# Performance work log

Measured on AMD Instinct MI355X. Metric: run time of the kernel, lower is better.

Reference implementation:

```python
import jax, jax.numpy as jnp
import numpy as np

K, D, N = 32, 128, 65536
EPS = 1e-6


def setup_inputs() -> dict:
    key = jax.random.key(0)
    k1, k2, k3 = jax.random.split(key, 3)
    x = jax.random.normal(k1, (N, D), dtype=jnp.float32)
    means = jax.random.normal(k2, (K, D), dtype=jnp.float32)
    # SPD covariances (original init is identity; use SPD perturbation so Cholesky is valid)
    B = jax.random.normal(k3, (K, D, D), dtype=jnp.float32) * 0.1
    covariances = jnp.einsum('kij,klj->kil', B, B) / D + jnp.eye(D, dtype=jnp.float32)
    weights = jnp.ones((K,), dtype=jnp.float32) / K
    return {"x": x, "means": means, "covariances": covariances, "weights": weights}


def reference(x, means, covariances, weights):
    d = x.shape[-1]
    cov = covariances + EPS * jnp.eye(d, dtype=x.dtype)          # [K,D,D]
    L = jnp.linalg.cholesky(cov)                                 # [K,D,D]
    diff = x[None, :, :] - means[:, None, :]                     # [K,N,D]
    # Mahalanobis via triangular solve: m = ||L^{-1}(x-mu)||^2
    sol = jax.scipy.linalg.solve_triangular(
        L, jnp.swapaxes(diff, 1, 2), lower=True)                 # [K,D,N]
    maha = jnp.sum(sol * sol, axis=1)                            # [K,N]
    half_logdet = jnp.sum(jnp.log(jnp.diagonal(L, axis1=1, axis2=2)), axis=1)  # [K]
    log_prob = (-0.5 * (d * jnp.log(2.0 * jnp.pi) + maha)
                - half_logdet[:, None])                          # [K,N]
    weighted = log_prob.T + jnp.log(weights)                     # [N,K]
    return jax.nn.logsumexp(weighted, axis=1)                    # [N]
```

## Files before the change

### kernel.cpp

```cpp
#include <hip/hip_runtime.h>
#include <hip/hip_bf16.h>
#include <math.h>

#define KCOMP 32
#define DDIM  128
#define NPTS  65536
#define GMM_EPS 1e-6f
#define SA 129
#define UFT 1280

typedef __attribute__((ext_vector_type(8)))  __bf16 bf16x8;
typedef __attribute__((ext_vector_type(16))) float  f32x16;

__device__ __forceinline__ unsigned short f2bf(float f){
  unsigned u = __builtin_bit_cast(unsigned, f);
  u = (u + 0x7FFFu + ((u >> 16) & 1u)) >> 16;
  return (unsigned short)u;
}
__device__ __forceinline__ float rlane(float v, int lsrc){
  return __builtin_bit_cast(float, __builtin_amdgcn_readlane(__builtin_bit_cast(int, v), lsrc));
}

__device__ __noinline__ float chol_inv32(float* __restrict__ Ab,
                                         float* __restrict__ Wb,
                                         const int c){
  float ar[32], lr[32], rd[32], s[32];
  #pragma unroll
  for(int i=0;i<32;i++) ar[i] = Ab[i*SA + c];
  float mydiag = 1.f;
  #pragma unroll
  for(int j=0;j<32;j++){
    float d   = rlane(ar[j], j);
    float rsd = rsqrtf(d);
    rd[j] = rsd;
    float Lcj  = ar[j]*rsd;
    lr[j] = (c>=j) ? Lcj : 0.f;
    if(c==j) mydiag = Lcj;
    float coef = Lcj*rsd;
    #pragma unroll
    for(int i=j+1;i<32;i++){
      float bij = rlane(ar[i], j);
      ar[i] = fmaf(-bij, coef, ar[i]);
    }
  }
  #pragma unroll
  for(int j=0;j<32;j++) Ab[c*SA + j] = lr[j];
  #pragma unroll
  for(int i=0;i<32;i++) s[i] = (i==c) ? 1.f : 0.f;
  #pragma unroll
  for(int j=0;j<32;j++){
    float vj = s[j]*rd[j];
    s[j] = vj;
    #pragma unroll
    for(int i=j+1;i<32;i++)
      s[i] = fmaf(-rlane(lr[j], i), vj, s[i]);
  }
  #pragma unroll
  for(int i=0;i<32;i++) Wb[i*SA + c] = s[i];
  return logf(mydiag);
}

__device__ __noinline__ void panel_unit(float* __restrict__ A, const float* __restrict__ W,
                                        int r0, int c0, int b, int ibl){
  const int b32=b*32;
  float acc[4][4]={};
  for(int kc=0;kc<32;kc+=4){
    float a_[4][4], b_[4][4];
    #pragma unroll
    for(int e=0;e<4;e++)
      #pragma unroll
      for(int g=0;g<4;g++){
        a_[e][g]=A[(32*ibl+r0+e)*SA + b32+kc+g];
        b_[e][g]=W[(b32+c0+e)*SA   + b32+kc+g];
      }
    #pragma unroll
    for(int e=0;e<4;e++)
      #pragma unroll
      for(int f=0;f<4;f++)
        acc[e][f]+=a_[e][0]*b_[f][0]+a_[e][1]*b_[f][1]
                  +a_[e][2]*b_[f][2]+a_[e][3]*b_[f][3];
  }
  #pragma unroll
  for(int e=0;e<4;e++)
    #pragma unroll
    for(int f=0;f<4;f++)
      A[(32*ibl+r0+e)*SA + b32+c0+f] = acc[e][f];
}

__device__ __noinline__ void syrk_unit(float* __restrict__ A,
                                       int r0, int c0, int b, int ui, int uj){
  const int b32=b*32;
  float acc[4][4]={};
  for(int kc=0;kc<32;kc+=4){
    float a_[4][4], b_[4][4];
    #pragma unroll
    for(int e=0;e<4;e++)
      #pragma unroll
      for(int g=0;g<4;g++){
        a_[e][g]=A[(32*ui+r0+e)*SA + b32+kc+g];
        b_[e][g]=A[(32*uj+c0+e)*SA + b32+kc+g];
      }
    #pragma unroll
    for(int e=0;e<4;e++)
      #pragma unroll
      for(int f=0;f<4;f++)
        acc[e][f]+=a_[e][0]*b_[f][0]+a_[e][1]*b_[f][1]
                  +a_[e][2]*b_[f][2]+a_[e][3]*b_[f][3];
  }
  #pragma unroll
  for(int e=0;e<4;e++)
    #pragma unroll
    for(int f=0;f<4;f++)
      A[(32*ui+r0+e)*SA+32*uj+c0+f] -= acc[e][f];
}

__device__ __noinline__ void tg_unit(const float* __restrict__ A, const float* __restrict__ W,
                                     float* __restrict__ T, int r0, int c0, int i, int j){
  float acc[4][4]={};
  #pragma unroll 1
  for(int p=j;p<i;p++){
    for(int kc=0;kc<32;kc+=4){
      float a_[4][4], b_[4][4];
      #pragma unroll
      for(int e=0;e<4;e++)
        #pragma unroll
        for(int g=0;g<4;g++){
          a_[e][g]=A[(32*i+r0+e)*SA + 32*p+kc+g];
          b_[e][g]=W[(32*p+kc+e)*SA + 32*j+c0+g];
        }
      #pragma unroll
      for(int e=0;e<4;e++)
        #pragma unroll
        for(int f=0;f<4;f++)
          acc[e][f]+=a_[e][0]*b_[0][f]+a_[e][1]*b_[1][f]
                    +a_[e][2]*b_[2][f]+a_[e][3]*b_[3][f];
    }
  }
  #pragma unroll
  for(int e=0;e<4;e++)
    #pragma unroll
    for(int f=0;f<4;f++)
      T[(r0+e)*33+c0+f]=acc[e][f];
}

__device__ __noinline__ void a2_unit(float* __restrict__ W, const float* __restrict__ T,
                                     int r0, int c0, int i, int j){
  float ac2[4][4]={};
  for(int kc=0;kc<32;kc+=4){
    float a_[4][4], b_[4][4];
    #pragma unroll
    for(int e=0;e<4;e++)
      #pragma unroll
      for(int g=0;g<4;g++){
        a_[e][g]=W[(32*i+r0+e)*SA + 32*i+kc+g];
        b_[e][g]=T[(kc+e)*33 + c0+g];
      }
    #pragma unroll
    for(int e=0;e<4;e++)
      #pragma unroll
      for(int f=0;f<4;f++)
        ac2[e][f]+=a_[e][0]*b_[0][f]+a_[e][1]*b_[1][f]
                  +a_[e][2]*b_[2][f]+a_[e][3]*b_[3][f];
  }
  #pragma unroll
  for(int e=0;e<4;e++)
    #pragma unroll
    for(int f=0;f<4;f++)
      W[(32*i+r0+e)*SA+32*j+c0+f] = -ac2[e][f];
}

__device__ __forceinline__ void pack_tile(const float* __restrict__ W,
                                          uint4* __restrict__ uf4, int tile, int l){
  int db = (tile<2)?0:((tile<6)?1:((tile<12)?2:3));
  int kc = tile - ((db==0)?0:((db==1)?2:((db==2)?6:12)));
  int row=db*32+(l&31), colb=kc*16+((l>>5)<<3);
  unsigned uu[4];
  #pragma unroll
  for(int h2=0;h2<4;h2++){
    unsigned lo=f2bf(W[row*SA+colb+2*h2]);
    unsigned hi=f2bf(W[row*SA+colb+2*h2+1]);
    uu[h2]=lo|(hi<<16);
  }
  uint4 wv; wv.x=uu[0]; wv.y=uu[1]; wv.z=uu[2]; wv.w=uu[3];
  uf4[tile*64 + l] = wv;
}

__global__ __launch_bounds__(256) void k_prep(const float* __restrict__ cov,
                                              const float* __restrict__ wts,
                                              const float* __restrict__ means,
                                              float* __restrict__ ws_c3,
                                              unsigned short* __restrict__ qfrag,
                                              unsigned short* __restrict__ ufrag){
  __shared__ float A[DDIM*SA];
  __shared__ float W[DDIM*SA];
  __shared__ float Tb[3*1056];
  __shared__ float muS[DDIM];
  __shared__ float mq[256];
  const int t=threadIdx.x, w=t>>6, l=t&63, k=blockIdx.x;
  const int r0=(l>>3)*4, c0=(l&7)*4;
  uint4* ufK = (uint4*)ufrag + (size_t)k*UFT;

  const float4* cv4 = (const float4*)(cov + (size_t)k*DDIM*DDIM);
  #pragma unroll
  for(int v=0; v<16; v++){
    int idx4 = t + 256*v; float4 f = cv4[idx4];
    int e = idx4*4; int i = e>>7; int j = e&127;
    float* d = &A[i*SA+j]; d[0]=f.x; d[1]=f.y; d[2]=f.z; d[3]=f.w;
  }
  for(int z=t; z<DDIM*SA; z+=256) W[z] = 0.f;
  if(t<DDIM) muS[t] = means[k*DDIM+t];
  __syncthreads();
  if(t<DDIM) A[t*SA+t] += GMM_EPS;
  __syncthreads();

  float hl = 0.f;
  if(w==0) hl += chol_inv32(&A[0], &W[0], l&31);
  __syncthreads();
  if(w==1)      panel_unit(A,W,r0,c0,0,1);
  else if(w==2) panel_unit(A,W,r0,c0,0,2);
  else if(w==3) panel_unit(A,W,r0,c0,0,3);
  __syncthreads();
  if(w==0)      syrk_unit(A,r0,c0,0,1,1);
  else if(w==1) syrk_unit(A,r0,c0,0,2,1);
  else if(w==2) syrk_unit(A,r0,c0,0,3,1);
  else          syrk_unit(A,r0,c0,0,2,2);
  __syncthreads();
  if(w==0)      hl += chol_inv32(&A[32*SA+32], &W[32*SA+32], l&31);
  else if(w==1) syrk_unit(A,r0,c0,0,3,2);
  else if(w==2) syrk_unit(A,r0,c0,0,3,3);
  __syncthreads();
  if(w==1)      panel_unit(A,W,r0,c0,1,2);
  else if(w==2) panel_unit(A,W,r0,c0,1,3);
  else if(w==3) tg_unit(A,W,&Tb[0],r0,c0,1,0);
  __syncthreads();
  if(w==0)      syrk_unit(A,r0,c0,1,2,2);
  else if(w==1) a2_unit(W,&Tb[0],r0,c0,1,0);
  else if(w==2) tg_unit(A,W,&Tb[1056],r0,c0,2,1);
  else          syrk_unit(A,r0,c0,1,3,2);
  __syncthreads();
  if(w==0)      hl += chol_inv32(&A[64*SA+64], &W[64*SA+64], l&31);
  else if(w==1) syrk_unit(A,r0,c0,1,3,3);
  else if(w==2) tg_unit(A,W,&Tb[0],r0,c0,2,0);
  __syncthreads();
  if(w==1)      panel_unit(A,W,r0,c0,2,3);
  else if(w==2) a2_unit(W,&Tb[0],r0,c0,2,0);
  else if(w==3) a2_unit(W,&Tb[1056],r0,c0,2,1);
  __syncthreads();
  if(w==0)      syrk_unit(A,r0,c0,2,3,3);
  else if(w==1) tg_unit(A,W,&Tb[0],r0,c0,3,0);
  else if(w==2) tg_unit(A,W,&Tb[1056],r0,c0,3,1);
  else          tg_unit(A,W,&Tb[2112],r0,c0,3,2);
  __syncthreads();
  if(w==0)      hl += chol_inv32(&A[96*SA+96], &W[96*SA+96], l&31);
  else if(w==1 || (w==2 && l<32)){
    int r = (w==1)? l : 64+l;
    float s=0.f;
    #pragma unroll 8
    for(int c=0;c<DDIM;c++) s += W[r*SA+c]*muS[c];
    mq[r]=s;
  }
  __syncthreads();
  if(w==1)      a2_unit(W,&Tb[0],r0,c0,3,0);
  else if(w==2) a2_unit(W,&Tb[1056],r0,c0,3,1);
  else if(w==3) a2_unit(W,&Tb[2112],r0,c0,3,2);
  __syncthreads();
  if(w==0){
    if(l<32){
      int r = 96+l;
      float s=0.f;
      #pragma unroll 8
      for(int c=0;c<DDIM;c++) s += W[r*SA+c]*muS[c];
      mq[r]=s;
    }
  } else {
    #pragma unroll
    for(int j=0;j<4;j++) pack_tile(W, ufK, (w-1)*4+j, l);
  }
  __syncthreads();
  if(t<128){
    float s=0.f;
    #pragma unroll 8
    for(int r=0;r<DDIM;r++) s += W[r*SA+t]*mq[r];
    mq[128+t]=s;
  } else if(w==2){
    #pragma unroll
    for(int j=0;j<4;j++) pack_tile(W, ufK, 12+j, l);
  } else {
    #pragma unroll
    for(int j=0;j<4;j++) pack_tile(W, ufK, 16+j, l);
  }
  __syncthreads();
  if(w==0){
    float hv = (l<32)? hl : 0.f;
    float p  = mq[l]*mq[l] + mq[l+64]*mq[l+64];
    #pragma unroll
    for(int off=32; off; off>>=1){ hv += __shfl_xor(hv,off); p += __shfl_xor(p,off); }
    if(l==0) ws_c3[k] = logf(wts[k]) - hv - 117.6241322f - 0.5f*p;
  } else if(w==1 && l<16){
    int tile=l>>1, half=l&1;
    const float* qq=&mq[128 + tile*16 + half*8];
    unsigned uu[4];
    #pragma unroll
    for(int h2=0;h2<4;h2++){
      unsigned lo=f2bf(qq[2*h2]), hi=f2bf(qq[2*h2+1]);
      uu[h2]=lo|(hi<<16);
    }
    uint4 wv; wv.x=uu[0]; wv.y=uu[1]; wv.z=uu[2]; wv.w=uu[3];
    ((uint4*)qfrag)[tile*64 + half*32 + k] = wv;
  }
}

#define MFMA_B(acc,u,xv) acc=__builtin_amdgcn_mfma_f32_32x32x16_bf16(__builtin_bit_cast(bf16x8,u),xv,acc,0,0,0)

__global__ __launch_bounds__(512,2) void k_main(const float* __restrict__ x,
                                                const uint4* __restrict__ uf,
                                                const uint4* __restrict__ qf,
                                                const float* __restrict__ ws_c3,
                                                float* __restrict__ out){
  __shared__ uint4 xs[4*8*64];
  __shared__ float lin[KCOMP*128];
  __shared__ float mahaS[4*8*128];
  __shared__ float c3s[KCOMP];
  const int t=threadIdx.x, lane=t&63, w=t>>6;
  const int qh=lane>>5, ln=lane&31;
  const size_t n0=(size_t)blockIdx.x*128;

  if(t<KCOMP) c3s[t]=ws_c3[t];

  {
    const float* xb = x + n0*DDIM;
    #pragma unroll
    for(int j=0;j<8;j++){
      int idx = j*512 + t;
      int n = idx & 127, d0 = (idx>>7)*4;
      float4 f = *(const float4*)(xb + (size_t)n*DDIM + d0);
      unsigned lo = f2bf(f.x) | (((unsigned)f2bf(f.y))<<16);
      unsigned hi = f2bf(f.z) | (((unsigned)f2bf(f.w))<<16);
      int tile=n>>5, lnn=n&31, c=d0>>4, qq=(d0>>3)&1, e4=d0&7;
      *(uint2*)((char*)xs + tile*8192 + c*1024 + qq*512 + lnn*16 + e4*2)
          = make_uint2(lo,hi);
    }
  }
  __syncthreads();

  if(w<4){
    f32x16 aq={};
    #pragma unroll
    for(int c=0;c<8;c++){
      uint4 qr = qf[c*64+lane];
      bf16x8 xq = __builtin_bit_cast(bf16x8, xs[w*512 + c*64 + lane]);
      MFMA_B(aq, qr, xq);
    }
    #pragma unroll
    for(int r=0;r<16;r++){
      int row=(r&3)+8*(r>>2)+4*qh;
      lin[row*128 + w*32 + ln] = -2.f*aq[r];
    }
  }

  #pragma unroll 1
  for(int iter=0;iter<4;iter++){
    const int k = iter*8 + w;
    uint4 ur[20];
    #pragma unroll
    for(int j=0;j<20;j++) ur[j]=uf[(size_t)k*UFT + j*64 + lane];

    #pragma unroll 1
    for(int tile=0;tile<4;tile++){
      bf16x8 xf[8];
      #pragma unroll
      for(int c=0;c<8;c++) xf[c]=__builtin_bit_cast(bf16x8, xs[tile*512 + c*64 + lane]);
      f32x16 a0={},a1={},a2={},a3={};
      #pragma unroll
      for(int c=0;c<2;c++) MFMA_B(a0, ur[c],    xf[c]);
      #pragma unroll
      for(int c=0;c<4;c++) MFMA_B(a1, ur[2+c],  xf[c]);
      #pragma unroll
      for(int c=0;c<6;c++) MFMA_B(a2, ur[6+c],  xf[c]);
      #pragma unroll
      for(int c=0;c<8;c++) MFMA_B(a3, ur[12+c], xf[c]);
      float p0=0.f,p1=0.f,p2=0.f,p3=0.f;
      #pragma unroll
      for(int r=0;r<16;r+=2){
        p0=fmaf(a0[r],a0[r],p0); p1=fmaf(a0[r+1],a0[r+1],p1);
        p2=fmaf(a1[r],a1[r],p2); p3=fmaf(a1[r+1],a1[r+1],p3);
        p0=fmaf(a2[r],a2[r],p0); p1=fmaf(a2[r+1],a2[r+1],p1);
        p2=fmaf(a3[r],a3[r],p2); p3=fmaf(a3[r+1],a3[r+1],p3);
      }
      float p=(p0+p1)+(p2+p3);
      p += __shfl_xor(p,32);
      if(qh==0) mahaS[iter*1024 + w*128 + tile*32 + ln] = p;
    }
  }
  __syncthreads();

  if(t<128){
    float m_run=-INFINITY, s_run=0.f;
    #pragma unroll 1
    for(int k3=0;k3<KCOMP;k3++){
      float a  = c3s[k3] - 0.5f*(mahaS[(k3>>3)*1024 + (k3&7)*128 + t] + lin[k3*128 + t]);
      float nm = fmaxf(m_run,a);
      s_run = s_run*__expf(m_run-nm)+__expf(a-nm);
      m_run = nm;
    }
    out[n0+t] = m_run + logf(s_run);
  }
}

extern "C" void kernel_launch(void* const* d_in, const int* in_sizes, int n_in,
                              void* d_out, int out_size, void* d_ws, size_t ws_size,
                              hipStream_t stream){
  const float* x   = (const float*)d_in[0];
  const float* mu  = (const float*)d_in[1];
  const float* cov = (const float*)d_in[2];
  const float* wts = (const float*)d_in[3];
  float* out = (float*)d_out;
  char*  ws  = (char*)d_ws;

  float*          wsC3 = (float*)ws;
  unsigned short* wsQF = (unsigned short*)(ws + 512);
  unsigned short* wsUF = (unsigned short*)(ws + 16384);

  k_prep<<<KCOMP, 256, 0, stream>>>(cov, wts, mu, wsC3, wsQF, wsUF);
  k_main<<<NPTS/128, 512, 0, stream>>>(x, (const uint4*)wsUF, (const uint4*)wsQF, wsC3, out);
}
```

Measured before the change: 174.4 us.

## Split per-component MFMA chains across wave pairs to halve register use

Each component's four triangular accumulator chains are now split between two waves: one wave handles the 2- and 8-chunk chains, the other the 4- and 6-chunk chains. This balances MFMA work and halves the preloaded U fragments per wave (10 instead of 20). Partial Mahalanobis sums are combined with shared-memory atomic adds into a zero-initialised buffer. Launch bounds are raised to 4 blocks per CU to increase occupancy. The trade-off is that U fragments are reloaded per component, shared atomics are added, and register pressure under the new bound may force spills.

```diff
diff --git a/kernel.cpp b/kernel.cpp
--- a/kernel.cpp
+++ b/kernel.cpp
@@ -312,20 +312,59 @@
 
 #define MFMA_B(acc,u,xv) acc=__builtin_amdgcn_mfma_f32_32x32x16_bf16(__builtin_bit_cast(bf16x8,u),xv,acc,0,0,0)
 
-__global__ __launch_bounds__(512,2) void k_main(const float* __restrict__ x,
+#define TM0(j) ((j)<2 ? (j) : (j)+10)
+#define TM1(j) ((j)+2)
+
+#define CLOOP(EA_, EB_, NF_, TM) {                                            \
+    _Pragma("unroll 1")                                                       \
+    for(int c8=0; c8<8; c8++){                                                \
+      const int k2 = g*8 + c8;                                                \
+      uint4 ur[10];                                                           \
+      const uint4* up = uf + (size_t)k2*UFT;                                  \
+      _Pragma("unroll")                                                       \
+      for(int j=0;j<10;j++) ur[j] = up[(size_t)(TM(j))*64 + lane];            \
+      _Pragma("unroll 1")                                                     \
+      for(int tile=0;tile<4;tile++){                                          \
+        bf16x8 xf[8];                                                         \
+        _Pragma("unroll")                                                     \
+        for(int c=0;c<NF_;c++) xf[c]=__builtin_bit_cast(bf16x8, xs[tile*512 + c*64 + lane]); \
+        f32x16 aA={}, aB={};                                                  \
+        _Pragma("unroll")                                                     \
+        for(int c=0;c<EA_;c++) MFMA_B(aA, ur[c], xf[c]);                      \
+        _Pragma("unroll")                                                     \
+        for(int c=0;c<EB_;c++) MFMA_B(aB, ur[EA_+c], xf[c]);                  \
+        float p0=0.f,p1=0.f;                                                  \
+        _Pragma("unroll")                                                     \
+        for(int r=0;r<16;r+=2){                                               \
+          p0=fmaf(aA[r],aA[r],p0);   p1=fmaf(aA[r+1],aA[r+1],p1);             \
+          p0=fmaf(aB[r],aB[r],p0);   p1=fmaf(aB[r+1],aB[r+1],p1);             \
+        }                                                                     \
+        float p=p0+p1;                                                        \
+        p += __shfl_xor(p,32);                                                \
+        if(qh==0) atomicAdd(&mahaS[k2*128 + tile*32 + ln], p);                \
+      }                                                                       \
+    }                                                                         \
+  }
+
+__global__ __launch_bounds__(512,4) void k_main(const float* __restrict__ x,
                                                 const uint4* __restrict__ uf,
                                                 const uint4* __restrict__ qf,
                                                 const float* __restrict__ ws_c3,
                                                 float* __restrict__ out){
   __shared__ uint4 xs[4*8*64];
   __shared__ float lin[KCOMP*128];
-  __shared__ float mahaS[4*8*128];
+  __shared__ float mahaS[KCOMP*128];
   __shared__ float c3s[KCOMP];
   const int t=threadIdx.x, lane=t&63, w=t>>6;
   const int qh=lane>>5, ln=lane&31;
+  const int sel=w&1, g=w>>1;
   const size_t n0=(size_t)blockIdx.x*128;
 
   if(t<KCOMP) c3s[t]=ws_c3[t];
+  {
+    float4 z={0.f,0.f,0.f,0.f};
+    float4* mz=(float4*)mahaS; mz[t]=z; mz[t+512]=z;
+  }
 
   {
     const float* xb = x + n0*DDIM;
@@ -344,12 +383,14 @@
   __syncthreads();
 
   if(w<4){
+    uint4 qr[8];
+    #pragma unroll
+    for(int c=0;c<8;c++) qr[c]=qf[c*64+lane];
     f32x16 aq={};
     #pragma unroll
     for(int c=0;c<8;c++){
-      uint4 qr = qf[c*64+lane];
       bf16x8 xq = __builtin_bit_cast(bf16x8, xs[w*512 + c*64 + lane]);
-      MFMA_B(aq, qr, xq);
+      MFMA_B(aq, qr[c], xq);
     }
     #pragma unroll
     for(int r=0;r<16;r++){
@@ -358,47 +399,14 @@
     }
   }
 
-  #pragma unroll 1
-  for(int iter=0;iter<4;iter++){
-    const int k = iter*8 + w;
-    uint4 ur[20];
-    #pragma unroll
-    for(int j=0;j<20;j++) ur[j]=uf[(size_t)k*UFT + j*64 + lane];
-
-    #pragma unroll 1
-    for(int tile=0;tile<4;tile++){
-      bf16x8 xf[8];
-      #pragma unroll
-      for(int c=0;c<8;c++) xf[c]=__builtin_bit_cast(bf16x8, xs[tile*512 + c*64 + lane]);
-      f32x16 a0={},a1={},a2={},a3={};
-      #pragma unroll
-      for(int c=0;c<2;c++) MFMA_B(a0, ur[c],    xf[c]);
-      #pragma unroll
-      for(int c=0;c<4;c++) MFMA_B(a1, ur[2+c],  xf[c]);
-      #pragma unroll
-      for(int c=0;c<6;c++) MFMA_B(a2, ur[6+c],  xf[c]);
-      #pragma unroll
-      for(int c=0;c<8;c++) MFMA_B(a3, ur[12+c], xf[c]);
-      float p0=0.f,p1=0.f,p2=0.f,p3=0.f;
-      #pragma unroll
-      for(int r=0;r<16;r+=2){
-        p0=fmaf(a0[r],a0[r],p0); p1=fmaf(a0[r+1],a0[r+1],p1);
-        p2=fmaf(a1[r],a1[r],p2); p3=fmaf(a1[r+1],a1[r+1],p3);
-        p0=fmaf(a2[r],a2[r],p0); p1=fmaf(a2[r+1],a2[r+1],p1);
-        p2=fmaf(a3[r],a3[r],p2); p3=fmaf(a3[r+1],a3[r+1],p3);
-      }
-      float p=(p0+p1)+(p2+p3);
-      p += __shfl_xor(p,32);
-      if(qh==0) mahaS[iter*1024 + w*128 + tile*32 + ln] = p;
-    }
-  }
+  if(sel==0){ CLOOP(2,8,8,TM0) } else { CLOOP(4,6,6,TM1) }
   __syncthreads();
 
   if(t<128){
     float m_run=-INFINITY, s_run=0.f;
     #pragma unroll 1
     for(int k3=0;k3<KCOMP;k3++){
-      float a  = c3s[k3] - 0.5f*(mahaS[(k3>>3)*1024 + (k3&7)*128 + t] + lin[k3*128 + t]);
+      float a  = c3s[k3] - 0.5f*(mahaS[k3*128 + t] + lin[k3*128 + t]);
       float nm = fmaxf(m_run,a);
       s_run = s_run*__expf(m_run-nm)+__expf(a-nm);
       m_run = nm;
```

Measured after the change: 176.8 us. No clear change (+1.3%).
